# Kernel tuning notes

Hardware: AMD Instinct MI355X
Metric: run time of the kernel (lower is better)

## Reference

```python
import jax, jax.numpy as jnp
import numpy as np

N = 100000
E = 1600000
D = 128
L = 3  # num_layers
EPS = 1e-5


def setup_inputs() -> dict:
    key = jax.random.key(0)
    ks = jax.random.split(key, 10)
    feat = jax.random.normal(ks[0], (N, D), dtype=jnp.float32)
    src = jax.random.randint(ks[1], (E,), 0, N, dtype=jnp.int32)
    dst = jax.random.randint(ks[2], (E,), 0, N, dtype=jnp.int32)
    s = 1.0 / np.sqrt(D)
    W_pool = jax.random.uniform(ks[3], (L, D, D), jnp.float32, -s, s)
    b_pool = jax.random.uniform(ks[4], (L, D), jnp.float32, -s, s)
    W_self = jax.random.uniform(ks[5], (L, D, D), jnp.float32, -s, s)
    W_neigh = jax.random.uniform(ks[6], (L, D, D), jnp.float32, -s, s)
    bias = jnp.zeros((L, D), jnp.float32)
    gamma = jnp.ones((L, D), jnp.float32)
    beta = jnp.zeros((L, D), jnp.float32)
    return {"feat": feat, "W_pool": W_pool, "b_pool": b_pool, "W_self": W_self,
            "W_neigh": W_neigh, "bias": bias, "gamma": gamma, "beta": beta,
            "src": src, "dst": dst}


def _sage_pool_layer(h, Wp, bp, Ws, Wn, b, src_all, dst_all):
    # DGL SAGEConv(aggregator_type='pool'):
    # h_pool = relu(fc_pool(h)); neigh = max over in-edges of h_pool[src];
    # out = fc_self(h) + fc_neigh(neigh) + bias  (fc_self/fc_neigh bias-free)
    hp = jax.nn.relu(h @ Wp + bp)                      # [N, d]
    msgs = hp[src_all]                                  # [E+N, d] gather
    neigh = jax.ops.segment_max(msgs, dst_all, num_segments=N)  # [N, d]
    return h @ Ws + neigh @ Wn + b


def _bn_relu(x, g, b):
    # BatchNorm1d in training mode (batch stats, biased variance) + ReLU
    mean = jnp.mean(x, axis=0)
    var = jnp.mean(jnp.square(x - mean), axis=0)
    return jax.nn.relu((x - mean) * jax.lax.rsqrt(var + EPS) * g + b)


def reference(feat, W_pool, b_pool, W_self, W_neigh, bias, gamma, beta, src, dst):
    # dgl.add_self_loop
    loop = jnp.arange(N, dtype=src.dtype)
    src_all = jnp.concatenate([src, loop])
    dst_all = jnp.concatenate([dst, loop])
    h = feat
    for l in range(L):
        h = _sage_pool_layer(h, W_pool[l], b_pool[l], W_self[l], W_neigh[l],
                             bias[l], src_all, dst_all)
        h = _bn_relu(h, gamma[l], beta[l])
    return h
```

## Files before the change

kernel.cpp:

```cpp
#include <hip/hip_runtime.h>

#define DD 128
#define MAXB 256
#define BSH 9
#define PEB 4096
#define RB 64

typedef unsigned short u16;
typedef unsigned int   u32;
typedef __attribute__((ext_vector_type(8))) short bf16x8;
typedef __attribute__((ext_vector_type(4))) float f32x4;

union U8 { uint4 u; bf16x8 v; };

__device__ inline u16 f2bf(float x) {
  u32 u = __float_as_uint(x);
  u += 0x7fffu + ((u >> 16) & 1u);
  return (u16)(u >> 16);
}
__device__ inline float bf2f_lo(u32 w) { return __uint_as_float(w << 16); }
__device__ inline float bf2f_hi(u32 w) { return __uint_as_float(w & 0xffff0000u); }

__device__ inline u32 pkmax(u32 a, u32 b) {
  u32 r;
  asm("v_pk_max_u16 %0, %1, %2" : "=v"(r) : "v"(a), "v"(b));
  return r;
}

__device__ inline uint4 fragF32(const float* __restrict__ p) {
  float4 a = *(const float4*)p;
  float4 b = *(const float4*)(p + 4);
  uint4 o;
  o.x = (u32)f2bf(a.x) | ((u32)f2bf(a.y) << 16);
  o.y = (u32)f2bf(a.z) | ((u32)f2bf(a.w) << 16);
  o.z = (u32)f2bf(b.x) | ((u32)f2bf(b.y) << 16);
  o.w = (u32)f2bf(b.z) | ((u32)f2bf(b.w) << 16);
  return o;
}

__device__ inline uint4 fragBN(const u16* __restrict__ p,
                               const float* __restrict__ sc,
                               const float* __restrict__ sh, int k0) {
  uint4 u = *(const uint4*)p;
  float4 c0 = *(const float4*)(sc + k0);
  float4 c1 = *(const float4*)(sc + k0 + 4);
  float4 h0 = *(const float4*)(sh + k0);
  float4 h1 = *(const float4*)(sh + k0 + 4);
  float y0 = fmaxf(fmaf(bf2f_lo(u.x), c0.x, h0.x), 0.f);
  float y1 = fmaxf(fmaf(bf2f_hi(u.x), c0.y, h0.y), 0.f);
  float y2 = fmaxf(fmaf(bf2f_lo(u.y), c0.z, h0.z), 0.f);
  float y3 = fmaxf(fmaf(bf2f_hi(u.y), c0.w, h0.w), 0.f);
  float y4 = fmaxf(fmaf(bf2f_lo(u.z), c1.x, h1.x), 0.f);
  float y5 = fmaxf(fmaf(bf2f_hi(u.z), c1.y, h1.y), 0.f);
  float y6 = fmaxf(fmaf(bf2f_lo(u.w), c1.z, h1.z), 0.f);
  float y7 = fmaxf(fmaf(bf2f_hi(u.w), c1.w, h1.w), 0.f);
  uint4 o;
  o.x = (u32)f2bf(y0) | ((u32)f2bf(y1) << 16);
  o.y = (u32)f2bf(y2) | ((u32)f2bf(y3) << 16);
  o.z = (u32)f2bf(y4) | ((u32)f2bf(y5) << 16);
  o.w = (u32)f2bf(y6) | ((u32)f2bf(y7) << 16);
  return o;
}

__global__ __launch_bounds__(256) void k_pack_w(
    const float* __restrict__ Wp, const float* __restrict__ Wsf,
    const float* __restrict__ Wn, u16* __restrict__ Wpk)
{
  int g = blockIdx.x * 256 + threadIdx.x;
  int m = g >> 11;
  if (m >= 9) return;
  int t = g & 2047;
  const float* W = (m < 3) ? Wp + (size_t)m * 16384
                 : (m < 6) ? Wsf + (size_t)(m - 3) * 16384
                           : Wn + (size_t)(m - 6) * 16384;
  int ks = t >> 9, nt = (t >> 6) & 7, l = t & 63;
  int kbase = ks * 32 + (l >> 4) * 8;
  int n = nt * 16 + (l & 15);
  u32 o[4];
#pragma unroll
  for (int p = 0; p < 4; p++) {
    u16 e0 = f2bf(W[(size_t)(kbase + 2 * p) * DD + n]);
    u16 e1 = f2bf(W[(size_t)(kbase + 2 * p + 1) * DD + n]);
    o[p] = (u32)e0 | ((u32)e1 << 16);
  }
  uint4* dst = (uint4*)(Wpk + (size_t)m * 16384 + (size_t)t * 8);
  *dst = make_uint4(o[0], o[1], o[2], o[3]);
}

template<int MODE>
__global__ __launch_bounds__(256, 4) void k_gemm_pool(
    const float* __restrict__ featf, const u16* __restrict__ xb,
    const u16* __restrict__ Wpk, const float* __restrict__ bvec,
    const float* __restrict__ sc, const float* __restrict__ sh,
    u16* __restrict__ hp, int nrows)
{
  const int tid = threadIdx.x;
  const int w = tid >> 6, l = tid & 63;
  const int lg = l >> 4, lm = l & 15;
  const int m0 = blockIdx.x * 128 + w * 32;

  f32x4 acc[2][8];
#pragma unroll
  for (int a = 0; a < 2; a++)
#pragma unroll
    for (int b = 0; b < 8; b++) acc[a][b] = (f32x4){0.f, 0.f, 0.f, 0.f};

  int n0 = m0 + lm;      if (n0 >= nrows) n0 = nrows - 1;
  int n1 = m0 + 16 + lm; if (n1 >= nrows) n1 = nrows - 1;
  const u16* wl = Wpk + l * 8;

#pragma unroll
  for (int ks = 0; ks < 4; ks++) {
    const int k0 = ks * 32 + lg * 8;
    U8 a0, a1;
    if (MODE == 0) {
      a0.u = fragF32(featf + (size_t)n0 * DD + k0);
      a1.u = fragF32(featf + (size_t)n1 * DD + k0);
    } else {
      a0.u = fragBN(xb + (size_t)n0 * DD + k0, sc, sh, k0);
      a1.u = fragBN(xb + (size_t)n1 * DD + k0, sc, sh, k0);
    }
#pragma unroll
    for (int nt = 0; nt < 8; nt++) {
      bf16x8 wf = *(const bf16x8*)(wl + (ks * 8 + nt) * 512);
      acc[0][nt] = __builtin_amdgcn_mfma_f32_16x16x32_bf16(wf, a0.v, acc[0][nt], 0, 0, 0);
      acc[1][nt] = __builtin_amdgcn_mfma_f32_16x16x32_bf16(wf, a1.v, acc[1][nt], 0, 0, 0);
    }
  }

#pragma unroll
  for (int mf = 0; mf < 2; mf++) {
    int node = m0 + mf * 16 + lm;
    if (node < nrows) {
      u16* dst = hp + (size_t)node * DD + lg * 4;
#pragma unroll
      for (int nt = 0; nt < 8; nt++) {
        float4 b4 = *(const float4*)(bvec + nt * 16 + lg * 4);
        f32x4 a = acc[mf][nt];
        float v0 = fmaxf(a[0] + b4.x, 0.f);
        float v1 = fmaxf(a[1] + b4.y, 0.f);
        float v2 = fmaxf(a[2] + b4.z, 0.f);
        float v3 = fmaxf(a[3] + b4.w, 0.f);
        uint2 o;
        o.x = (u32)f2bf(v0) | ((u32)f2bf(v1) << 16);
        o.y = (u32)f2bf(v2) | ((u32)f2bf(v3) << 16);
        *(uint2*)(dst + nt * 16) = o;
      }
    }
  }
}

template<int MODE>
__global__ __launch_bounds__(256, 4) void k_gemm_out(
    const float* __restrict__ featf, u16* xb,
    const u16* __restrict__ gb,
    const u16* __restrict__ WpkS, const u16* __restrict__ WpkN,
    const float* __restrict__ bvec,
    const float* __restrict__ sc, const float* __restrict__ sh,
    float* __restrict__ parts, int nrows)
{
  __shared__ float red[64 * 132];
  const int tid = threadIdx.x;
  const int w = tid >> 6, l = tid & 63;
  const int lg = l >> 4, lm = l & 15;
  const int m0 = blockIdx.x * 128 + w * 32;

  f32x4 acc[2][8];
#pragma unroll
  for (int a = 0; a < 2; a++)
#pragma unroll
    for (int b = 0; b < 8; b++) acc[a][b] = (f32x4){0.f, 0.f, 0.f, 0.f};

  int n0 = m0 + lm;      if (n0 >= nrows) n0 = nrows - 1;
  int n1 = m0 + 16 + lm; if (n1 >= nrows) n1 = nrows - 1;

#pragma unroll
  for (int ks = 0; ks < 4; ks++) {
    const int k0 = ks * 32 + lg * 8;
    U8 a0, a1;
    if (MODE == 0) {
      a0.u = fragF32(featf + (size_t)n0 * DD + k0);
      a1.u = fragF32(featf + (size_t)n1 * DD + k0);
    } else {
      a0.u = fragBN(xb + (size_t)n0 * DD + k0, sc, sh, k0);
      a1.u = fragBN(xb + (size_t)n1 * DD + k0, sc, sh, k0);
    }
    const u16* wl = WpkS + l * 8;
#pragma unroll
    for (int nt = 0; nt < 8; nt++) {
      bf16x8 wf = *(const bf16x8*)(wl + (ks * 8 + nt) * 512);
      acc[0][nt] = __builtin_amdgcn_mfma_f32_16x16x32_bf16(wf, a0.v, acc[0][nt], 0, 0, 0);
      acc[1][nt] = __builtin_amdgcn_mfma_f32_16x16x32_bf16(wf, a1.v, acc[1][nt], 0, 0, 0);
    }
  }
#pragma unroll
  for (int ks = 0; ks < 4; ks++) {
    const int k0 = ks * 32 + lg * 8;
    bf16x8 g0 = *(const bf16x8*)(gb + (size_t)n0 * DD + k0);
    bf16x8 g1 = *(const bf16x8*)(gb + (size_t)n1 * DD + k0);
    const u16* wl = WpkN + l * 8;
#pragma unroll
    for (int nt = 0; nt < 8; nt++) {
      bf16x8 wf = *(const bf16x8*)(wl + (ks * 8 + nt) * 512);
      acc[0][nt] = __builtin_amdgcn_mfma_f32_16x16x32_bf16(wf, g0, acc[0][nt], 0, 0, 0);
      acc[1][nt] = __builtin_amdgcn_mfma_f32_16x16x32_bf16(wf, g1, acc[1][nt], 0, 0, 0);
    }
  }

  const float msk0 = (m0 + lm < nrows) ? 1.f : 0.f;
  const float msk1 = (m0 + 16 + lm < nrows) ? 1.f : 0.f;
#pragma unroll
  for (int nt = 0; nt < 8; nt++) {
    float4 b4 = *(const float4*)(bvec + nt * 16 + lg * 4);
    acc[0][nt][0] += b4.x; acc[0][nt][1] += b4.y;
    acc[0][nt][2] += b4.z; acc[0][nt][3] += b4.w;
    acc[1][nt][0] += b4.x; acc[1][nt][1] += b4.y;
    acc[1][nt][2] += b4.z; acc[1][nt][3] += b4.w;
  }
#pragma unroll
  for (int mf = 0; mf < 2; mf++) {
    int node = m0 + mf * 16 + lm;
    if (node < nrows) {
      u16* dst = xb + (size_t)node * DD + lg * 4;
#pragma unroll
      for (int nt = 0; nt < 8; nt++) {
        f32x4 a = acc[mf][nt];
        uint2 o;
        o.x = (u32)f2bf(a[0]) | ((u32)f2bf(a[1]) << 16);
        o.y = (u32)f2bf(a[2]) | ((u32)f2bf(a[3]) << 16);
        *(uint2*)(dst + nt * 16) = o;
      }
    }
  }

  const int rowbase = (w * 16 + lm) * 132;
#pragma unroll
  for (int nt = 0; nt < 8; nt++) {
    float4 sv;
    sv.x = msk0 * acc[0][nt][0] + msk1 * acc[1][nt][0];
    sv.y = msk0 * acc[0][nt][1] + msk1 * acc[1][nt][1];
    sv.z = msk0 * acc[0][nt][2] + msk1 * acc[1][nt][2];
    sv.w = msk0 * acc[0][nt][3] + msk1 * acc[1][nt][3];
    *(float4*)&red[rowbase + nt * 16 + lg * 4] = sv;
  }
  __syncthreads();
  float ssum = 0.f;
  if (tid < 128) {
#pragma unroll
    for (int r = 0; r < 64; r++) ssum += red[r * 132 + tid];
  }
  __syncthreads();
#pragma unroll
  for (int nt = 0; nt < 8; nt++) {
    float4 qv;
    qv.x = msk0 * acc[0][nt][0] * acc[0][nt][0] + msk1 * acc[1][nt][0] * acc[1][nt][0];
    qv.y = msk0 * acc[0][nt][1] * acc[0][nt][1] + msk1 * acc[1][nt][1] * acc[1][nt][1];
    qv.z = msk0 * acc[0][nt][2] * acc[0][nt][2] + msk1 * acc[1][nt][2] * acc[1][nt][2];
    qv.w = msk0 * acc[0][nt][3] * acc[0][nt][3] + msk1 * acc[1][nt][3] * acc[1][nt][3];
    *(float4*)&red[rowbase + nt * 16 + lg * 4] = qv;
  }
  __syncthreads();
  if (tid < 128) {
    float qsum = 0.f;
#pragma unroll
    for (int r = 0; r < 64; r++) qsum += red[r * 132 + tid];
    parts[(size_t)blockIdx.x * 256 + tid] = ssum;
    parts[(size_t)blockIdx.x * 256 + 128 + tid] = qsum;
  }
}

__global__ __launch_bounds__(256) void k_red1(
    const float* __restrict__ parts, float* __restrict__ pp, int nblk)
{
  int t = threadIdx.x;
  float s = 0.f;
  for (int r = blockIdx.x; r < nblk; r += RB) s += parts[(size_t)r * 256 + t];
  pp[blockIdx.x * 256 + t] = s;
}

__global__ __launch_bounds__(256) void k_zero_i(int* p, int n) {
  int i = blockIdx.x * 256 + threadIdx.x;
  if (i < n) p[i] = 0;
}

__global__ __launch_bounds__(256) void k_histb(
    const int* __restrict__ dst, int* __restrict__ bcnt, int E)
{
  __shared__ int cnt[MAXB];
  const int e0 = blockIdx.x * PEB;
  const int e1 = min(e0 + PEB, E);
  for (int i = threadIdx.x; i < MAXB; i += 256) cnt[i] = 0;
  __syncthreads();
  for (int e = e0 + threadIdx.x; e < e1; e += 256)
    atomicAdd(&cnt[dst[e] >> BSH], 1);
  __syncthreads();
  for (int i = threadIdx.x; i < MAXB; i += 256)
    if (cnt[i]) atomicAdd(&bcnt[i], cnt[i]);
}

__global__ __launch_bounds__(256) void k_bscan(
    const int* __restrict__ bcnt, int* __restrict__ boff,
    int* __restrict__ bcur, int nbuk, int E)
{
  __shared__ int sm[256];
  int t = threadIdx.x;
  int v = (t < nbuk) ? bcnt[t] : 0;
  sm[t] = v;
  __syncthreads();
  int acc = v;
#pragma unroll
  for (int s = 1; s < 256; s <<= 1) {
    int u = (t >= s) ? sm[t - s] : 0;
    __syncthreads();
    acc += u;
    sm[t] = acc;
    __syncthreads();
  }
  if (t < nbuk) { boff[t] = acc - v; bcur[t] = acc - v; }
  if (t == 0) boff[nbuk] = E;
}

__global__ __launch_bounds__(256) void k_part(
    const int* __restrict__ src, const int* __restrict__ dst,
    int* __restrict__ bcur, int2* __restrict__ pairs, int E)
{
  __shared__ int cnt[MAXB];
  __shared__ int base[MAXB];
  const int e0 = blockIdx.x * PEB;
  const int e1 = min(e0 + PEB, E);
  for (int i = threadIdx.x; i < MAXB; i += 256) cnt[i] = 0;
  __syncthreads();
  for (int e = e0 + threadIdx.x; e < e1; e += 256)
    atomicAdd(&cnt[dst[e] >> BSH], 1);
  __syncthreads();
  for (int i = threadIdx.x; i < MAXB; i += 256) {
    int c = cnt[i];
    base[i] = c ? atomicAdd(&bcur[i], c) : 0;
    cnt[i] = 0;
  }
  __syncthreads();
  for (int e = e0 + threadIdx.x; e < e1; e += 256) {
    int d = dst[e], s = src[e];
    int b = d >> BSH;
    int r = atomicAdd(&cnt[b], 1);
    pairs[base[b] + r] = make_int2(s, d);
  }
}

__global__ __launch_bounds__(256) void k_csr(
    const int2* __restrict__ pairs, const int* __restrict__ boff,
    int* __restrict__ off, int* __restrict__ eidx, int nrows, int nbuk)
{
  __shared__ int cnt[512];
  __shared__ int ps[256];
  const int b = blockIdx.x;
  const int lo = boff[b], hi = boff[b + 1];
  const int t = threadIdx.x;
  cnt[t] = 0; cnt[t + 256] = 0;
  __syncthreads();
  for (int i = lo + t; i < hi; i += 256)
    atomicAdd(&cnt[pairs[i].y & 511], 1);
  __syncthreads();
  int c0 = cnt[2 * t], c1 = cnt[2 * t + 1];
  ps[t] = c0 + c1;
  __syncthreads();
  int acc = ps[t];
#pragma unroll
  for (int s = 1; s < 256; s <<= 1) {
    int u = (t >= s) ? ps[t - s] : 0;
    __syncthreads();
    acc += u;
    ps[t] = acc;
    __syncthreads();
  }
  int base = lo + acc - (c0 + c1);
  int node0 = (b << BSH) + 2 * t;
  if (node0 < nrows)     off[node0]     = base;
  if (node0 + 1 < nrows) off[node0 + 1] = base + c0;
  if (b == nbuk - 1 && t == 0) off[nrows] = hi;
  cnt[2 * t]     = base;
  cnt[2 * t + 1] = base + c0;
  __syncthreads();
  for (int i = lo + t; i < hi; i += 256) {
    int2 p = pairs[i];
    int pos = atomicAdd(&cnt[p.y & 511], 1);
    eidx[pos] = p.x;
  }
}

__global__ __launch_bounds__(256) void k_aggregate(
    const uint4* __restrict__ hp4, const int* __restrict__ off,
    const int* __restrict__ eidx, uint4* __restrict__ nb4, int nrows)
{
  int d = blockIdx.x * 4 + (threadIdx.x >> 6);
  if (d >= nrows) return;
  const int l = threadIdx.x & 63;
  const int part = l & 15;
  const int slot = l >> 4;
  uint4 a = hp4[(size_t)d * 16 + part];
  const int e = off[d + 1];
  int i = off[d] + slot;
  for (; i + 4 < e; i += 8) {
    int s0 = eidx[i];
    int s1 = eidx[i + 4];
    uint4 v0 = hp4[(size_t)s0 * 16 + part];
    uint4 v1 = hp4[(size_t)s1 * 16 + part];
    a.x = pkmax(a.x, pkmax(v0.x, v1.x));
    a.y = pkmax(a.y, pkmax(v0.y, v1.y));
    a.z = pkmax(a.z, pkmax(v0.z, v1.z));
    a.w = pkmax(a.w, pkmax(v0.w, v1.w));
  }
  if (i < e) {
    int s0 = eidx[i];
    uint4 v0 = hp4[(size_t)s0 * 16 + part];
    a.x = pkmax(a.x, v0.x); a.y = pkmax(a.y, v0.y);
    a.z = pkmax(a.z, v0.z); a.w = pkmax(a.w, v0.w);
  }
  a.x = pkmax(a.x, (u32)__shfl_xor((int)a.x, 16, 64));
  a.y = pkmax(a.y, (u32)__shfl_xor((int)a.y, 16, 64));
  a.z = pkmax(a.z, (u32)__shfl_xor((int)a.z, 16, 64));
  a.w = pkmax(a.w, (u32)__shfl_xor((int)a.w, 16, 64));
  a.x = pkmax(a.x, (u32)__shfl_xor((int)a.x, 32, 64));
  a.y = pkmax(a.y, (u32)__shfl_xor((int)a.y, 32, 64));
  a.z = pkmax(a.z, (u32)__shfl_xor((int)a.z, 32, 64));
  a.w = pkmax(a.w, (u32)__shfl_xor((int)a.w, 32, 64));
  if (slot == 0) nb4[(size_t)d * 16 + part] = a;
}

__global__ __launch_bounds__(256) void k_bn_prep(
    const float* __restrict__ pp,
    const float* __restrict__ gamma, const float* __restrict__ beta,
    float* __restrict__ sc, float* __restrict__ sh, float invN)
{
  __shared__ float sums[256];
  int t = threadIdx.x;
  float s = 0.f;
#pragma unroll
  for (int k = 0; k < RB; k++) s += pp[k * 256 + t];
  sums[t] = s;
  __syncthreads();
  if (t < 128) {
    float mean = sums[t] * invN;
    float var  = sums[128 + t] * invN - mean * mean;
    float g = gamma[t] * rsqrtf(var + 1e-5f);
    sc[t] = g;
    sh[t] = beta[t] - mean * g;
  }
}

__global__ __launch_bounds__(256) void k_bn_final(
    const u16* __restrict__ xb, float* __restrict__ out,
    const float* __restrict__ sc, const float* __restrict__ sh, int n8)
{
  int i = blockIdx.x * 256 + threadIdx.x;
  if (i >= n8) return;
  uint4 v = ((const uint4*)xb)[i];
  int f0 = (i & 15) * 8;
  float4 c0 = *(const float4*)(sc + f0);
  float4 c1 = *(const float4*)(sc + f0 + 4);
  float4 h0 = *(const float4*)(sh + f0);
  float4 h1 = *(const float4*)(sh + f0 + 4);
  float4* o = (float4*)out + 2 * (size_t)i;
  o[0] = make_float4(fmaxf(fmaf(bf2f_lo(v.x), c0.x, h0.x), 0.f),
                     fmaxf(fmaf(bf2f_hi(v.x), c0.y, h0.y), 0.f),
                     fmaxf(fmaf(bf2f_lo(v.y), c0.z, h0.z), 0.f),
                     fmaxf(fmaf(bf2f_hi(v.y), c0.w, h0.w), 0.f));
  o[1] = make_float4(fmaxf(fmaf(bf2f_lo(v.z), c1.x, h1.x), 0.f),
                     fmaxf(fmaf(bf2f_hi(v.z), c1.y, h1.y), 0.f),
                     fmaxf(fmaf(bf2f_lo(v.w), c1.z, h1.z), 0.f),
                     fmaxf(fmaf(bf2f_hi(v.w), c1.w, h1.w), 0.f));
}

extern "C" void kernel_launch(void* const* d_in, const int* in_sizes, int n_in,
                              void* d_out, int out_size, void* d_ws, size_t ws_size,
                              hipStream_t stream)
{
  const float* feat    = (const float*)d_in[0];
  const float* W_pool  = (const float*)d_in[1];
  const float* b_pool  = (const float*)d_in[2];
  const float* W_self  = (const float*)d_in[3];
  const float* W_neigh = (const float*)d_in[4];
  const float* bias    = (const float*)d_in[5];
  const float* gamma   = (const float*)d_in[6];
  const float* beta    = (const float*)d_in[7];
  const int*   src     = (const int*)d_in[8];
  const int*   dst     = (const int*)d_in[9];

  const int Nn = in_sizes[0] / DD;
  const int E  = in_sizes[8];
  float* out = (float*)d_out;

  const int gB = (Nn + 127) / 128;

  const size_t ND = (size_t)Nn * DD;
  u16*   xb    = (u16*)d_ws;
  u16*   hp    = xb + ND;
  u16*   nbuf  = hp + ND;
  u16*   Wpk   = nbuf + ND;
  float* sc    = (float*)(Wpk + 9 * 16384);
  float* sh    = sc + 128;
  float* pp    = sh + 128;
  float* parts = pp + RB * 256;
  int*   bcnt  = (int*)(parts + (size_t)gB * 256);
  int*   off   = bcnt + MAXB;
  int*   boff  = off + Nn + 2;
  int*   bcur  = boff + MAXB + 2;
  int2*  pairs = (int2*)(bcur + MAXB);
  int*   eidx  = (int*)(pairs + E);

  const int nbuk = (Nn + 511) >> BSH;
  const int pB   = (E + PEB - 1) / PEB;
  const int aggB = (Nn + 3) / 4;
  const int n8   = Nn * (DD / 8);
  const int cB   = (n8 + 255) / 256;

  k_pack_w<<<72, 256, 0, stream>>>(W_pool, W_self, W_neigh, Wpk);
  k_zero_i<<<1, 256, 0, stream>>>(bcnt, MAXB);
  k_histb<<<pB, 256, 0, stream>>>(dst, bcnt, E);
  k_bscan<<<1, 256, 0, stream>>>(bcnt, boff, bcur, nbuk, E);
  k_part<<<pB, 256, 0, stream>>>(src, dst, bcur, pairs, E);
  k_csr<<<nbuk, 256, 0, stream>>>(pairs, boff, off, eidx, Nn, nbuk);

  for (int l = 0; l < 3; l++) {
    const float* bp = b_pool + (size_t)l * DD;
    const float* bl = bias + (size_t)l * DD;
    const u16* WP = Wpk + (size_t)l * 16384;
    const u16* WS = Wpk + (size_t)(3 + l) * 16384;
    const u16* WN = Wpk + (size_t)(6 + l) * 16384;

    if (l == 0)
      k_gemm_pool<0><<<gB, 256, 0, stream>>>(feat, nullptr, WP, bp, sc, sh, hp, Nn);
    else
      k_gemm_pool<1><<<gB, 256, 0, stream>>>(nullptr, xb, WP, bp, sc, sh, hp, Nn);

    k_aggregate<<<aggB, 256, 0, stream>>>((const uint4*)hp, off, eidx, (uint4*)nbuf, Nn);

    if (l == 0)
      k_gemm_out<0><<<gB, 256, 0, stream>>>(feat, xb, nbuf, WS, WN, bl, sc, sh, parts, Nn);
    else
      k_gemm_out<1><<<gB, 256, 0, stream>>>(nullptr, xb, nbuf, WS, WN, bl, sc, sh, parts, Nn);

    k_red1<<<RB, 256, 0, stream>>>(parts, pp, gB);
    k_bn_prep<<<1, 256, 0, stream>>>(pp, gamma + (size_t)l * DD,
                                     beta + (size_t)l * DD, sc, sh, 1.0f / (float)Nn);
  }
  k_bn_final<<<cB, 256, 0, stream>>>(xb, out, sc, sh, n8);
  (void)n_in; (void)out_size; (void)ws_size;
}
```

Measured before the change: 452.5 us.

## Slice pooled features into column-sliced layout for cache-local max aggregation

The pooled activations and the aggregated neighbor buffer are stored as eight 16-column slices, each contiguous over all nodes. Aggregation blocks now handle one slice at a time, so the gathered working set per slice (about 3.2 MB) can stay in cache across random source indices. The GEMM epilogue and the neighbor-GEMM loads are changed to match the sliced layout. Edge pairs are also packed into one 32-bit word to halve partitioning traffic. The tradeoff is that each edge index is read eight times and every gather fetches only 32 bytes.

```diff
diff --git a/kernel.cpp b/kernel.cpp
--- a/kernel.cpp
+++ b/kernel.cpp
@@ -92,7 +92,7 @@
     const float* __restrict__ featf, const u16* __restrict__ xb,
     const u16* __restrict__ Wpk, const float* __restrict__ bvec,
     const float* __restrict__ sc, const float* __restrict__ sh,
-    u16* __restrict__ hp, int nrows)
+    u32* __restrict__ hp32, int nrows)
 {
   const int tid = threadIdx.x;
   const int w = tid >> 6, l = tid & 63;
@@ -132,7 +132,6 @@
   for (int mf = 0; mf < 2; mf++) {
     int node = m0 + mf * 16 + lm;
     if (node < nrows) {
-      u16* dst = hp + (size_t)node * DD + lg * 4;
 #pragma unroll
       for (int nt = 0; nt < 8; nt++) {
         float4 b4 = *(const float4*)(bvec + nt * 16 + lg * 4);
@@ -144,7 +143,7 @@
         uint2 o;
         o.x = (u32)f2bf(v0) | ((u32)f2bf(v1) << 16);
         o.y = (u32)f2bf(v2) | ((u32)f2bf(v3) << 16);
-        *(uint2*)(dst + nt * 16) = o;
+        *(uint2*)(hp32 + ((size_t)nt * nrows + node) * 8 + lg * 2) = o;
       }
     }
   }
@@ -195,9 +194,10 @@
   }
 #pragma unroll
   for (int ks = 0; ks < 4; ks++) {
-    const int k0 = ks * 32 + lg * 8;
-    bf16x8 g0 = *(const bf16x8*)(gb + (size_t)n0 * DD + k0);
-    bf16x8 g1 = *(const bf16x8*)(gb + (size_t)n1 * DD + k0);
+    const int sl = 2 * ks + (lg >> 1);
+    const int so = (lg & 1) * 8;
+    bf16x8 g0 = *(const bf16x8*)(gb + ((size_t)sl * nrows + n0) * 16 + so);
+    bf16x8 g1 = *(const bf16x8*)(gb + ((size_t)sl * nrows + n1) * 16 + so);
     const u16* wl = WpkN + l * 8;
 #pragma unroll
     for (int nt = 0; nt < 8; nt++) {
@@ -322,7 +322,7 @@
 
 __global__ __launch_bounds__(256) void k_part(
     const int* __restrict__ src, const int* __restrict__ dst,
-    int* __restrict__ bcur, int2* __restrict__ pairs, int E)
+    int* __restrict__ bcur, u32* __restrict__ pairs, int E)
 {
   __shared__ int cnt[MAXB];
   __shared__ int base[MAXB];
@@ -343,12 +343,12 @@
     int d = dst[e], s = src[e];
     int b = d >> BSH;
     int r = atomicAdd(&cnt[b], 1);
-    pairs[base[b] + r] = make_int2(s, d);
+    pairs[base[b] + r] = ((u32)s << 9) | (u32)(d & 511);
   }
 }
 
 __global__ __launch_bounds__(256) void k_csr(
-    const int2* __restrict__ pairs, const int* __restrict__ boff,
+    const u32* __restrict__ pairs, const int* __restrict__ boff,
     int* __restrict__ off, int* __restrict__ eidx, int nrows, int nbuk)
 {
   __shared__ int cnt[512];
@@ -359,7 +359,7 @@
   cnt[t] = 0; cnt[t + 256] = 0;
   __syncthreads();
   for (int i = lo + t; i < hi; i += 256)
-    atomicAdd(&cnt[pairs[i].y & 511], 1);
+    atomicAdd(&cnt[pairs[i] & 511], 1);
   __syncthreads();
   int c0 = cnt[2 * t], c1 = cnt[2 * t + 1];
   ps[t] = c0 + c1;
@@ -382,49 +382,49 @@
   cnt[2 * t + 1] = base + c0;
   __syncthreads();
   for (int i = lo + t; i < hi; i += 256) {
-    int2 p = pairs[i];
-    int pos = atomicAdd(&cnt[p.y & 511], 1);
-    eidx[pos] = p.x;
+    u32 p = pairs[i];
+    int pos = atomicAdd(&cnt[p & 511], 1);
+    eidx[pos] = (int)(p >> 9);
   }
 }
 
 __global__ __launch_bounds__(256) void k_aggregate(
-    const uint4* __restrict__ hp4, const int* __restrict__ off,
-    const int* __restrict__ eidx, uint4* __restrict__ nb4, int nrows)
-{
-  int d = blockIdx.x * 4 + (threadIdx.x >> 6);
+    const u32* __restrict__ hp, const int* __restrict__ off,
+    const int* __restrict__ eidx, u32* __restrict__ nb, int nrows)
+{
+  const int bid = blockIdx.x;
+  const int slice = bid & 7;
+  const int chunk = bid >> 3;
+  const int tid = threadIdx.x;
+  const int w = tid >> 6, l = tid & 63;
+  const int nq = l >> 4;
+  const int epar = (l >> 3) & 1;
+  const int dw = l & 7;
+  const int d = chunk * 16 + w * 4 + nq;
   if (d >= nrows) return;
-  const int l = threadIdx.x & 63;
-  const int part = l & 15;
-  const int slot = l >> 4;
-  uint4 a = hp4[(size_t)d * 16 + part];
-  const int e = off[d + 1];
-  int i = off[d] + slot;
-  for (; i + 4 < e; i += 8) {
-    int s0 = eidx[i];
-    int s1 = eidx[i + 4];
-    uint4 v0 = hp4[(size_t)s0 * 16 + part];
-    uint4 v1 = hp4[(size_t)s1 * 16 + part];
-    a.x = pkmax(a.x, pkmax(v0.x, v1.x));
-    a.y = pkmax(a.y, pkmax(v0.y, v1.y));
-    a.z = pkmax(a.z, pkmax(v0.z, v1.z));
-    a.w = pkmax(a.w, pkmax(v0.w, v1.w));
-  }
-  if (i < e) {
-    int s0 = eidx[i];
-    uint4 v0 = hp4[(size_t)s0 * 16 + part];
-    a.x = pkmax(a.x, v0.x); a.y = pkmax(a.y, v0.y);
-    a.z = pkmax(a.z, v0.z); a.w = pkmax(a.w, v0.w);
-  }
-  a.x = pkmax(a.x, (u32)__shfl_xor((int)a.x, 16, 64));
-  a.y = pkmax(a.y, (u32)__shfl_xor((int)a.y, 16, 64));
-  a.z = pkmax(a.z, (u32)__shfl_xor((int)a.z, 16, 64));
-  a.w = pkmax(a.w, (u32)__shfl_xor((int)a.w, 16, 64));
-  a.x = pkmax(a.x, (u32)__shfl_xor((int)a.x, 32, 64));
-  a.y = pkmax(a.y, (u32)__shfl_xor((int)a.y, 32, 64));
-  a.z = pkmax(a.z, (u32)__shfl_xor((int)a.z, 32, 64));
-  a.w = pkmax(a.w, (u32)__shfl_xor((int)a.w, 32, 64));
-  if (slot == 0) nb4[(size_t)d * 16 + part] = a;
+
+  const u32* __restrict__ base = hp + (size_t)slice * nrows * 8;
+  u32 a = base[(size_t)d * 8 + dw];
+  const int b = off[d], e = off[d + 1];
+  int p = b + epar;
+  for (; p + 6 < e; p += 8) {
+    int s0 = __builtin_nontemporal_load(eidx + p);
+    int s1 = __builtin_nontemporal_load(eidx + p + 2);
+    int s2 = __builtin_nontemporal_load(eidx + p + 4);
+    int s3 = __builtin_nontemporal_load(eidx + p + 6);
+    u32 v0 = base[(size_t)s0 * 8 + dw];
+    u32 v1 = base[(size_t)s1 * 8 + dw];
+    u32 v2 = base[(size_t)s2 * 8 + dw];
+    u32 v3 = base[(size_t)s3 * 8 + dw];
+    a = pkmax(pkmax(a, pkmax(v0, v1)), pkmax(v2, v3));
+  }
+  for (; p < e; p += 2) {
+    int s0 = __builtin_nontemporal_load(eidx + p);
+    a = pkmax(a, base[(size_t)s0 * 8 + dw]);
+  }
+  a = pkmax(a, (u32)__shfl_xor((int)a, 8, 64));
+  if (epar == 0)
+    nb[(size_t)slice * nrows * 8 + (size_t)d * 8 + dw] = a;
 }
 
 __global__ __launch_bounds__(256) void k_bn_prep(
@@ -505,12 +505,12 @@
   int*   off   = bcnt + MAXB;
   int*   boff  = off + Nn + 2;
   int*   bcur  = boff + MAXB + 2;
-  int2*  pairs = (int2*)(bcur + MAXB);
+  u32*   pairs = (u32*)(bcur + MAXB);
   int*   eidx  = (int*)(pairs + E);
 
   const int nbuk = (Nn + 511) >> BSH;
   const int pB   = (E + PEB - 1) / PEB;
-  const int aggB = (Nn + 3) / 4;
+  const int aggB = 8 * ((Nn + 15) / 16);
   const int n8   = Nn * (DD / 8);
   const int cB   = (n8 + 255) / 256;
 
@@ -529,11 +529,11 @@
     const u16* WN = Wpk + (size_t)(6 + l) * 16384;
 
     if (l == 0)
-      k_gemm_pool<0><<<gB, 256, 0, stream>>>(feat, nullptr, WP, bp, sc, sh, hp, Nn);
+      k_gemm_pool<0><<<gB, 256, 0, stream>>>(feat, nullptr, WP, bp, sc, sh, (u32*)hp, Nn);
     else
-      k_gemm_pool<1><<<gB, 256, 0, stream>>>(nullptr, xb, WP, bp, sc, sh, hp, Nn);
-
-    k_aggregate<<<aggB, 256, 0, stream>>>((const uint4*)hp, off, eidx, (uint4*)nbuf, Nn);
+      k_gemm_pool<1><<<gB, 256, 0, stream>>>(nullptr, xb, WP, bp, sc, sh, (u32*)hp, Nn);
+
+    k_aggregate<<<aggB, 256, 0, stream>>>((const u32*)hp, off, eidx, (u32*)nbuf, Nn);
 
     if (l == 0)
       k_gemm_out<0><<<gB, 256, 0, stream>>>(feat, xb, nbuf, WS, WN, bl, sc, sh, parts, Nn);
```

New measurement: 691.9 us. 1.53x slower.
